# Kernel tuning notes

Measured on AMD Instinct MI355X. Metric: run time of the kernel, lower is better.

## Reference

```python
import jax, jax.numpy as jnp
import numpy as np

B = 16384          # tokens
H = 2048           # hidden_size
E = 8              # num_experts
K = 2              # top-k
HF = H // 4        # expert bottleneck dim


def setup_inputs() -> dict:
    key = jax.random.key(0)
    k0, k1, k2, k3 = jax.random.split(key, 4)
    scale = lambda kk, shape, fan: jax.random.normal(kk, shape, jnp.float32) * (1.0 / np.sqrt(fan))
    x = jax.random.normal(k0, (B, H), jnp.float32)
    W1 = scale(k1, (E, H, HF), H)      # experts[e][0].weight (transposed)
    b1 = jnp.zeros((E, HF), jnp.float32)
    W2 = scale(k2, (E, HF), HF)        # experts[e][2].weight (out dim 1, no bias)
    Wg = scale(k3, (H, E), H)          # gate.weight (transposed)
    bg = jnp.zeros((E,), jnp.float32)
    return {"x": x, "W1": W1, "b1": b1, "W2": W2, "Wg": Wg, "bg": bg}


def reference(x, W1, b1, W2, Wg, bg):
    # Gating (eval mode: no noise branch)
    logits = x @ Wg + bg                                  # [B, E]
    top_w, top_i = jax.lax.top_k(logits, K)               # [B, K]
    w = jax.nn.softmax(top_w, axis=-1)                    # [B, K]
    # Scatter top-k softmax weights into dense combine weights [B, E];
    # unselected experts get weight 0, so the dense all-expert compute
    # below is mathematically identical to the masked dispatch loop.
    combine = jnp.zeros_like(logits).at[jnp.arange(x.shape[0])[:, None], top_i].add(w)
    # All-expert MLP: Linear -> exact GELU -> Linear(->1, no bias)
    h = jax.nn.gelu(jnp.einsum('bh,ehf->bef', x, W1) + b1, approximate=False)  # [B, E, HF]
    o = jnp.einsum('bef,ef->be', h, W2)                   # [B, E]
    final_scores = jnp.sum(combine * o, axis=-1, keepdims=True)  # [B, 1]
    return final_scores, logits
```

## Files before the change

### kernel.cpp

```cpp
#include <hip/hip_runtime.h>
#include <math.h>

#define B_TOK 16384
#define H_DIM 2048
#define NE    8
#define TOPK  2
#define HFD   512

#define TM 64
#define BK 32
#define NKSTEP (H_DIM / BK)

static constexpr size_t OFF_COUNTS = 0;
static constexpr size_t OFF_BUCKET = 1024;
static constexpr size_t OFF_WSLOT  = OFF_BUCKET + (size_t)NE * B_TOK * 4;
static constexpr size_t OFF_ROUTE  = OFF_WSLOT + (size_t)B_TOK * 2 * 4;
static constexpr size_t OFF_WGT    = 720896;
static constexpr size_t OFF_W1TS   = 1u << 20;
static constexpr size_t OFF_XB     = OFF_W1TS + (size_t)NE * HFD * H_DIM * 2;

typedef short bfrag __attribute__((ext_vector_type(8)));
typedef float facc  __attribute__((ext_vector_type(16)));

__device__ inline unsigned short f2bf(float f) {
    union { float f; unsigned u; } v; v.f = f;
    unsigned r = v.u + 0x7FFFu + ((v.u >> 16) & 1u);
    return (unsigned short)(r >> 16);
}
__device__ inline unsigned pack2(float lo, float hi) {
    return (unsigned)f2bf(lo) | ((unsigned)f2bf(hi) << 16);
}

__device__ __forceinline__ void gload_lds16(const void* g, void* l) {
    __builtin_amdgcn_global_load_lds(
        (const __attribute__((address_space(1))) unsigned int*)g,
        (__attribute__((address_space(3))) unsigned int*)l, 16, 0, 0);
}

__global__ __launch_bounds__(256)
void wg_transpose_kernel(const float* __restrict__ Wg,
                         float* __restrict__ WgT)
{
    const int t = threadIdx.x;
    #pragma unroll
    for (int rep = 0; rep < H_DIM / 256; ++rep) {
        const int h = rep * 256 + t;
        const float4 a = *reinterpret_cast<const float4*>(Wg + (size_t)h * NE);
        const float4 b = *reinterpret_cast<const float4*>(Wg + (size_t)h * NE + 4);
        WgT[0 * H_DIM + h] = a.x;  WgT[1 * H_DIM + h] = a.y;
        WgT[2 * H_DIM + h] = a.z;  WgT[3 * H_DIM + h] = a.w;
        WgT[4 * H_DIM + h] = b.x;  WgT[5 * H_DIM + h] = b.y;
        WgT[6 * H_DIM + h] = b.z;  WgT[7 * H_DIM + h] = b.w;
    }
}

__global__ __launch_bounds__(256)
void prep_w1_kernel(const float* __restrict__ W1,
                    unsigned short* __restrict__ W1ts)
{
    const int blk   = blockIdx.x;
    const int e     = blk >> 6;
    const int kstep = blk & 63;
    const int tid   = threadIdx.x;

    const float* src = W1 + ((size_t)e * H_DIM + kstep * BK) * HFD;
    unsigned short* dst = W1ts + (size_t)e * (HFD * H_DIM) + (size_t)kstep * (BK * HFD);

    #pragma unroll
    for (int s = 0; s < 4; ++s) {
        #pragma unroll
        for (int fh = 0; fh < 2; ++fh) {
            const int f = fh * 256 + tid;
            float v[8];
            #pragma unroll
            for (int j = 0; j < 8; ++j)
                v[j] = src[(size_t)(s * 8 + j) * HFD + f];
            uint4 p;
            p.x = pack2(v[0], v[1]); p.y = pack2(v[2], v[3]);
            p.z = pack2(v[4], v[5]); p.w = pack2(v[6], v[7]);
            *reinterpret_cast<uint4*>(dst + s * 4096 + f * 8) = p;
        }
    }
}

__global__ __launch_bounds__(256)
void gate_logits_kernel(const float* __restrict__ x,
                        const float* __restrict__ WgT,
                        const float* __restrict__ bg,
                        float* __restrict__ out_logits,
                        float* __restrict__ wslot,
                        int*   __restrict__ route,
                        unsigned short* __restrict__ xb)
{
    const int tok  = (blockIdx.x * blockDim.x + threadIdx.x) >> 6;
    const int lane = threadIdx.x & 63;
    if (tok >= B_TOK) return;

    const float* xrow = x + (size_t)tok * H_DIM;
    unsigned short* xbrow = xb + (size_t)tok * H_DIM;

    float acc[NE];
    #pragma unroll
    for (int e = 0; e < NE; ++e) acc[e] = 0.f;

    #pragma unroll 2
    for (int i = 0; i < H_DIM / 256; ++i) {
        const int h = i * 256 + 4 * lane;
        const float4 xv = *reinterpret_cast<const float4*>(xrow + h);
        uint2 p;
        p.x = pack2(xv.x, xv.y);
        p.y = pack2(xv.z, xv.w);
        *reinterpret_cast<uint2*>(xbrow + h) = p;
        #pragma unroll
        for (int e = 0; e < NE; ++e) {
            const float4 wv = *reinterpret_cast<const float4*>(WgT + (size_t)e * H_DIM + h);
            acc[e] += xv.x * wv.x + xv.y * wv.y + xv.z * wv.z + xv.w * wv.w;
        }
    }

    #pragma unroll
    for (int e = 0; e < NE; ++e) {
        #pragma unroll
        for (int off = 32; off > 0; off >>= 1)
            acc[e] += __shfl_xor(acc[e], off, 64);
    }

    if (lane == 0) {
        #pragma unroll
        for (int e = 0; e < NE; ++e) acc[e] += bg[e];

        float4* lo = reinterpret_cast<float4*>(out_logits + (size_t)tok * NE);
        lo[0] = make_float4(acc[0], acc[1], acc[2], acc[3]);
        lo[1] = make_float4(acc[4], acc[5], acc[6], acc[7]);

        int i0 = 0; float v0 = acc[0];
        #pragma unroll
        for (int e = 1; e < NE; ++e)
            if (acc[e] > v0) { v0 = acc[e]; i0 = e; }
        int i1 = -1; float v1 = -3.4e38f;
        #pragma unroll
        for (int e = 0; e < NE; ++e)
            if (e != i0 && acc[e] > v1) { v1 = acc[e]; i1 = e; }

        const float w0 = 1.f / (1.f + expf(v1 - v0));
        wslot[tok * 2]     = w0;
        wslot[tok * 2 + 1] = 1.f - w0;
        route[tok] = i0 | (i1 << 8);
    }
}

__global__ __launch_bounds__(1024)
void route_kernel(const int* __restrict__ route,
                  int* __restrict__ counts,
                  int* __restrict__ bucket)
{
    __shared__ int lcnt[NE];
    __shared__ int lbase[NE];
    const int tid = threadIdx.x;
    const int tok = blockIdx.x * 1024 + tid;

    if (tid < NE) lcnt[tid] = 0;
    __syncthreads();

    const int rt = route[tok];
    const int i0 = rt & 255;
    const int i1 = rt >> 8;
    const int r0 = atomicAdd(&lcnt[i0], 1);
    const int r1 = atomicAdd(&lcnt[i1], 1);
    __syncthreads();

    if (tid < NE) lbase[tid] = atomicAdd(&counts[tid], lcnt[tid]);
    __syncthreads();

    bucket[i0 * B_TOK + lbase[i0] + r0] = tok * 2;
    bucket[i1 * B_TOK + lbase[i1] + r1] = tok * 2 + 1;
}

__global__ __launch_bounds__(512, 4)
void expert_mfma_kernel(const unsigned short* __restrict__ xb,
                        const unsigned short* __restrict__ W1ts,
                        const float* __restrict__ b1,
                        const float* __restrict__ W2,
                        const int*   __restrict__ counts,
                        const int*   __restrict__ bucket,
                        const float* __restrict__ wslot,
                        float* __restrict__ out_scores)
{
    const int e = blockIdx.x & 7;
    const int t = blockIdx.x >> 3;
    const int n = counts[e];
    const int start = t * TM;
    if (start >= n) return;
    const int nt = min(TM, n - start);

    __shared__ unsigned short Abuf[2][4 * 4096];
    __shared__ unsigned short Xbuf[2][4 * 512];
    __shared__ float o_part[8][TM];

    const int tid = threadIdx.x;
    const int w   = tid >> 6;
    const int l   = tid & 63;
    const int lo5 = l & 31;
    const int hi  = l >> 5;

    const unsigned short* W1e = W1ts + (size_t)e * (HFD * H_DIM);

    const unsigned short* xsrc = nullptr;
    if (w < 4) {
        const int ent = bucket[e * B_TOK + start + min(l, nt - 1)];
        xsrc = xb + (size_t)(ent >> 1) * H_DIM + w * 8;
    }

    facc acc[2][2];
    #pragma unroll
    for (int m = 0; m < 2; ++m)
        #pragma unroll
        for (int nb = 0; nb < 2; ++nb)
            #pragma unroll
            for (int r = 0; r < 16; ++r) acc[m][nb][r] = 0.f;

    #define STAGE(KK, BUF) do {                                               \
        const unsigned short* asrc_ = W1e + (size_t)(KK) * (BK * HFD);        \
        const int c0_ = w * 4;                                                \
        gload_lds16(asrc_ + (c0_ + 0) * 512 + l * 8, &Abuf[BUF][(c0_ + 0) * 512 + l * 8]); \
        gload_lds16(asrc_ + (c0_ + 1) * 512 + l * 8, &Abuf[BUF][(c0_ + 1) * 512 + l * 8]); \
        gload_lds16(asrc_ + (c0_ + 2) * 512 + l * 8, &Abuf[BUF][(c0_ + 2) * 512 + l * 8]); \
        gload_lds16(asrc_ + (c0_ + 3) * 512 + l * 8, &Abuf[BUF][(c0_ + 3) * 512 + l * 8]); \
        if (w < 4) gload_lds16(xsrc + (size_t)(KK) * BK, &Xbuf[BUF][w * 512 + l * 8]);     \
    } while (0)

    STAGE(0, 0);

    for (int kk = 0; kk < NKSTEP; ++kk) {
        const int cur = kk & 1;
        if (kk < NKSTEP - 1) {
            STAGE(kk + 1, cur ^ 1);
            if (w < 4) asm volatile("s_waitcnt vmcnt(5)" ::: "memory");
            else       asm volatile("s_waitcnt vmcnt(4)" ::: "memory");
        } else {
            asm volatile("s_waitcnt vmcnt(0)" ::: "memory");
        }
        __builtin_amdgcn_s_barrier();

        #pragma unroll
        for (int ks = 0; ks < 2; ++ks) {
            const int slot = ks * 2 + hi;
            const bfrag a0 = *reinterpret_cast<const bfrag*>(
                &Abuf[cur][slot * 4096 + (w * 64 + lo5) * 8]);
            const bfrag a1 = *reinterpret_cast<const bfrag*>(
                &Abuf[cur][slot * 4096 + (w * 64 + 32 + lo5) * 8]);
            const bfrag b0 = *reinterpret_cast<const bfrag*>(
                &Xbuf[cur][slot * 512 + lo5 * 8]);
            const bfrag b1f = *reinterpret_cast<const bfrag*>(
                &Xbuf[cur][slot * 512 + (32 + lo5) * 8]);
            acc[0][0] = __builtin_amdgcn_mfma_f32_32x32x16_bf16(a0, b0,  acc[0][0], 0, 0, 0);
            acc[0][1] = __builtin_amdgcn_mfma_f32_32x32x16_bf16(a0, b1f, acc[0][1], 0, 0, 0);
            acc[1][0] = __builtin_amdgcn_mfma_f32_32x32x16_bf16(a1, b0,  acc[1][0], 0, 0, 0);
            acc[1][1] = __builtin_amdgcn_mfma_f32_32x32x16_bf16(a1, b1f, acc[1][1], 0, 0, 0);
        }
        __builtin_amdgcn_s_barrier();
    }
    #undef STAGE

    const float* b1e = b1 + e * HFD;
    const float* W2e = W2 + e * HFD;
    const float kInvSqrt2 = 0.70710678118654752f;

    float po0 = 0.f, po1 = 0.f;
    #pragma unroll
    for (int m = 0; m < 2; ++m) {
        const int base = w * 64 + m * 32 + 4 * hi;
        #pragma unroll
        for (int r = 0; r < 16; ++r) {
            const int frow = base + (r & 3) + 8 * (r >> 2);
            const float bv = b1e[frow];
            const float wv = W2e[frow];
            const float h0 = acc[m][0][r] + bv;
            const float h1 = acc[m][1][r] + bv;
            po0 += 0.5f * h0 * (1.f + erff(h0 * kInvSqrt2)) * wv;
            po1 += 0.5f * h1 * (1.f + erff(h1 * kInvSqrt2)) * wv;
        }
    }
    po0 += __shfl_xor(po0, 32, 64);
    po1 += __shfl_xor(po1, 32, 64);

    if (hi == 0) {
        o_part[w][lo5]      = po0;
        o_part[w][32 + lo5] = po1;
    }
    __syncthreads();

    if (tid < nt) {
        const int entry = bucket[e * B_TOK + start + tid];
        float o = 0.f;
        #pragma unroll
        for (int w8 = 0; w8 < 8; ++w8) o += o_part[w8][tid];
        atomicAdd(&out_scores[entry >> 1], wslot[entry] * o);
    }
}

extern "C" void kernel_launch(void* const* d_in, const int* in_sizes, int n_in,
                              void* d_out, int out_size, void* d_ws, size_t ws_size,
                              hipStream_t stream)
{
    const float* x  = (const float*)d_in[0];
    const float* W1 = (const float*)d_in[1];
    const float* b1 = (const float*)d_in[2];
    const float* W2 = (const float*)d_in[3];
    const float* Wg = (const float*)d_in[4];
    const float* bg = (const float*)d_in[5];

    float* out        = (float*)d_out;
    float* out_scores = out;
    float* out_logits = out + B_TOK;

    char* ws = (char*)d_ws;
    int*            counts = (int*)           (ws + OFF_COUNTS);
    int*            bucket = (int*)           (ws + OFF_BUCKET);
    float*          wslot  = (float*)         (ws + OFF_WSLOT);
    int*            route  = (int*)           (ws + OFF_ROUTE);
    float*          WgT    = (float*)         (ws + OFF_WGT);
    unsigned short* W1ts   = (unsigned short*)(ws + OFF_W1TS);
    unsigned short* xb     = (unsigned short*)(ws + OFF_XB);

    hipMemsetAsync(counts, 0, NE * sizeof(int), stream);
    hipMemsetAsync(out_scores, 0, B_TOK * sizeof(float), stream);

    wg_transpose_kernel<<<1, 256, 0, stream>>>(Wg, WgT);

    prep_w1_kernel<<<NE * NKSTEP, 256, 0, stream>>>(W1, W1ts);

    gate_logits_kernel<<<B_TOK / 4, 256, 0, stream>>>(x, WgT, bg, out_logits,
                                                      wslot, route, xb);

    route_kernel<<<B_TOK / 1024, 1024, 0, stream>>>(route, counts, bucket);

    expert_mfma_kernel<<<NE * (B_TOK / TM), 512, 0, stream>>>(
        xb, W1ts, b1, W2, counts, bucket, wslot, out_scores);
}
```

Baseline: 299.8 us.

## Double token tile to 128 with 3-stage LDS pipeline and 4x2 MFMA warp tiles

Doubles the per-block token tile so each W1 tile loaded into LDS is reused across twice as many tokens, halving weight traffic per token. Warps now cover 128 hidden features by 64 tokens (4x2 MFMA accumulators) instead of 64x64, and the global-to-LDS prefetch goes from two-stage to three-stage with adjusted vmcnt waits. It also raises wave priority around the MFMA block. More accumulators and LDS lower occupancy (launch bounds 4 to 2), and larger tiles waste more work on partially filled expert buckets.

```diff
diff --git a/kernel.cpp b/kernel.cpp
--- a/kernel.cpp
+++ b/kernel.cpp
@@ -7,9 +7,10 @@
 #define TOPK  2
 #define HFD   512
 
-#define TM 64
+#define TM 128
 #define BK 32
 #define NKSTEP (H_DIM / BK)
+#define NSTAGE 3
 
 static constexpr size_t OFF_COUNTS = 0;
 static constexpr size_t OFF_BUCKET = 1024;
@@ -176,7 +177,7 @@
     bucket[i1 * B_TOK + lbase[i1] + r1] = tok * 2 + 1;
 }
 
-__global__ __launch_bounds__(512, 4)
+__global__ __launch_bounds__(512, 2)
 void expert_mfma_kernel(const unsigned short* __restrict__ xb,
                         const unsigned short* __restrict__ W1ts,
                         const float* __restrict__ b1,
@@ -193,27 +194,33 @@
     if (start >= n) return;
     const int nt = min(TM, n - start);
 
-    __shared__ unsigned short Abuf[2][4 * 4096];
-    __shared__ unsigned short Xbuf[2][4 * 512];
-    __shared__ float o_part[8][TM];
+    __shared__ unsigned short Abuf[NSTAGE][4 * HFD * 8];
+    __shared__ unsigned short Xbuf[NSTAGE][4 * TM * 8];
+    __shared__ float o_part[4][TM];
 
     const int tid = threadIdx.x;
     const int w   = tid >> 6;
     const int l   = tid & 63;
     const int lo5 = l & 31;
     const int hi  = l >> 5;
+    const int fr  = w & 3;
+    const int tg  = w >> 2;
 
     const unsigned short* W1e = W1ts + (size_t)e * (HFD * H_DIM);
 
-    const unsigned short* xsrc = nullptr;
-    if (w < 4) {
-        const int ent = bucket[e * B_TOK + start + min(l, nt - 1)];
-        xsrc = xb + (size_t)(ent >> 1) * H_DIM + w * 8;
-    }
-
-    facc acc[2][2];
-    #pragma unroll
-    for (int m = 0; m < 2; ++m)
+    const int sx   = w & 3;
+    const int th   = w >> 2;
+    const int xtok = th * 64 + l;
+    const int xent = bucket[e * B_TOK + start + min(xtok, nt - 1)];
+    const unsigned short* xsrc = xb + (size_t)(xent >> 1) * H_DIM + sx * 8;
+    unsigned short* xdst_base[NSTAGE];
+    #pragma unroll
+    for (int s = 0; s < NSTAGE; ++s)
+        xdst_base[s] = &Xbuf[s][(sx * TM + xtok) * 8];
+
+    facc acc[4][2];
+    #pragma unroll
+    for (int m = 0; m < 4; ++m)
         #pragma unroll
         for (int nb = 0; nb < 2; ++nb)
             #pragma unroll
@@ -226,39 +233,49 @@
         gload_lds16(asrc_ + (c0_ + 1) * 512 + l * 8, &Abuf[BUF][(c0_ + 1) * 512 + l * 8]); \
         gload_lds16(asrc_ + (c0_ + 2) * 512 + l * 8, &Abuf[BUF][(c0_ + 2) * 512 + l * 8]); \
         gload_lds16(asrc_ + (c0_ + 3) * 512 + l * 8, &Abuf[BUF][(c0_ + 3) * 512 + l * 8]); \
-        if (w < 4) gload_lds16(xsrc + (size_t)(KK) * BK, &Xbuf[BUF][w * 512 + l * 8]);     \
+        gload_lds16(xsrc + (size_t)(KK) * BK, xdst_base[BUF]);                \
     } while (0)
 
     STAGE(0, 0);
-
+    STAGE(1, 1);
+
+    int cur = 0;
     for (int kk = 0; kk < NKSTEP; ++kk) {
-        const int cur = kk & 1;
-        if (kk < NKSTEP - 1) {
-            STAGE(kk + 1, cur ^ 1);
-            if (w < 4) asm volatile("s_waitcnt vmcnt(5)" ::: "memory");
-            else       asm volatile("s_waitcnt vmcnt(4)" ::: "memory");
+        if (kk + 2 < NKSTEP) {
+            const int sb = (cur + 2 >= NSTAGE) ? (cur + 2 - NSTAGE) : (cur + 2);
+            STAGE(kk + 2, sb);
+            asm volatile("s_waitcnt vmcnt(10)" ::: "memory");
+        } else if (kk + 1 < NKSTEP) {
+            asm volatile("s_waitcnt vmcnt(5)" ::: "memory");
         } else {
             asm volatile("s_waitcnt vmcnt(0)" ::: "memory");
         }
         __builtin_amdgcn_s_barrier();
 
+        __builtin_amdgcn_s_setprio(1);
         #pragma unroll
         for (int ks = 0; ks < 2; ++ks) {
             const int slot = ks * 2 + hi;
-            const bfrag a0 = *reinterpret_cast<const bfrag*>(
-                &Abuf[cur][slot * 4096 + (w * 64 + lo5) * 8]);
-            const bfrag a1 = *reinterpret_cast<const bfrag*>(
-                &Abuf[cur][slot * 4096 + (w * 64 + 32 + lo5) * 8]);
-            const bfrag b0 = *reinterpret_cast<const bfrag*>(
-                &Xbuf[cur][slot * 512 + lo5 * 8]);
-            const bfrag b1f = *reinterpret_cast<const bfrag*>(
-                &Xbuf[cur][slot * 512 + (32 + lo5) * 8]);
-            acc[0][0] = __builtin_amdgcn_mfma_f32_32x32x16_bf16(a0, b0,  acc[0][0], 0, 0, 0);
-            acc[0][1] = __builtin_amdgcn_mfma_f32_32x32x16_bf16(a0, b1f, acc[0][1], 0, 0, 0);
-            acc[1][0] = __builtin_amdgcn_mfma_f32_32x32x16_bf16(a1, b0,  acc[1][0], 0, 0, 0);
-            acc[1][1] = __builtin_amdgcn_mfma_f32_32x32x16_bf16(a1, b1f, acc[1][1], 0, 0, 0);
-        }
+            bfrag a[4], bb[2];
+            #pragma unroll
+            for (int m = 0; m < 4; ++m)
+                a[m] = *reinterpret_cast<const bfrag*>(
+                    &Abuf[cur][(slot * 512 + fr * 128 + m * 32 + lo5) * 8]);
+            #pragma unroll
+            for (int nb = 0; nb < 2; ++nb)
+                bb[nb] = *reinterpret_cast<const bfrag*>(
+                    &Xbuf[cur][(slot * TM + tg * 64 + nb * 32 + lo5) * 8]);
+            #pragma unroll
+            for (int m = 0; m < 4; ++m)
+                #pragma unroll
+                for (int nb = 0; nb < 2; ++nb)
+                    acc[m][nb] = __builtin_amdgcn_mfma_f32_32x32x16_bf16(
+                        a[m], bb[nb], acc[m][nb], 0, 0, 0);
+        }
+        __builtin_amdgcn_s_setprio(0);
         __builtin_amdgcn_s_barrier();
+
+        cur = (cur + 1 >= NSTAGE) ? 0 : cur + 1;
     }
     #undef STAGE
 
@@ -268,8 +285,8 @@
 
     float po0 = 0.f, po1 = 0.f;
     #pragma unroll
-    for (int m = 0; m < 2; ++m) {
-        const int base = w * 64 + m * 32 + 4 * hi;
+    for (int m = 0; m < 4; ++m) {
+        const int base = fr * 128 + m * 32 + 4 * hi;
         #pragma unroll
         for (int r = 0; r < 16; ++r) {
             const int frow = base + (r & 3) + 8 * (r >> 2);
@@ -285,16 +302,15 @@
     po1 += __shfl_xor(po1, 32, 64);
 
     if (hi == 0) {
-        o_part[w][lo5]      = po0;
-        o_part[w][32 + lo5] = po1;
+        o_part[fr][tg * 64 + lo5]      = po0;
+        o_part[fr][tg * 64 + 32 + lo5] = po1;
     }
     __syncthreads();
 
     if (tid < nt) {
         const int entry = bucket[e * B_TOK + start + tid];
-        float o = 0.f;
-        #pragma unroll
-        for (int w8 = 0; w8 < 8; ++w8) o += o_part[w8][tid];
+        const float o = o_part[0][tid] + o_part[1][tid]
+                      + o_part[2][tid] + o_part[3][tid];
         atomicAdd(&out_scores[entry >> 1], wslot[entry] * o);
     }
 }
```

Measured after the change: 392.8 us. 1.31x slower.
